# Optimization experiments

Measured on AMD Instinct MI355X. Metric: run time of the kernel, lower is better.

## Reference

```python
import jax, jax.numpy as jnp
import numpy as np

B, S, D, H = 2, 2048, 2048, 16
HD = D // H  # 128


def setup_inputs() -> dict:
    key = jax.random.key(0)
    ks = jax.random.split(key, 5)
    scale = 0.02
    return {
        "hidden_states": jax.random.normal(ks[0], (B, S, D), dtype=jnp.float32),
        "Wqkv_w": jax.random.normal(ks[1], (3 * D, D), dtype=jnp.float32) * scale,
        "Wqkv_b": jax.random.normal(ks[2], (3 * D,), dtype=jnp.float32) * scale,
        "out_w": jax.random.normal(ks[3], (D, D), dtype=jnp.float32) * scale,
        "out_b": jax.random.normal(ks[4], (D,), dtype=jnp.float32) * scale,
    }


def reference(hidden_states, Wqkv_w, Wqkv_b, out_w, out_b):
    b, s, d = hidden_states.shape
    # QKV projection (torch Linear: x @ W.T + b)
    qkv = hidden_states @ Wqkv_w.T + Wqkv_b          # [b, s, 3d]
    qkv = qkv.reshape(b, s, 3, H, HD)                 # 'b s (three h d)'
    q, k, v = qkv[:, :, 0], qkv[:, :, 1], qkv[:, :, 2]  # [b, s, h, hd]
    softmax_scale = 1.0 / np.float32(np.sqrt(HD))
    # full quadratic scores, matching the naive baddbmm path
    scores = jnp.einsum('bthd,bshd->bhts', q, k) * softmax_scale  # [b,h,t,s]
    # causal=False (module default), dropout_p=0.0 -> no mask, no dropout
    attn = jax.nn.softmax(scores, axis=-1)
    ctx = jnp.einsum('bhts,bshd->bthd', attn, v)      # [b, t, h, hd]
    ctx = ctx.reshape(b, s, d)
    return ctx @ out_w.T + out_b
```

## Files before the change

### kernel.cpp

```cpp
#include <hip/hip_runtime.h>
#include <cstdint>
#include <cstddef>

#define B_ 2
#define S_ 2048
#define D_ 2048
#define H_ 16
#define HD_ 128
#define NTOK 4096
#define NQKV 6144

typedef unsigned short u16;
typedef __attribute__((ext_vector_type(8))) __bf16 bf16x8;
typedef __attribute__((ext_vector_type(4))) float f32x4;

__device__ __forceinline__ u16 f2bf(float f) {
  uint32_t u = __builtin_bit_cast(uint32_t, f);
  u = (u + 0x7FFFu + ((u >> 16) & 1u)) >> 16;
  return (u16)u;
}

__device__ __forceinline__ void gload_lds16(const void* g, void* l) {
  __builtin_amdgcn_global_load_lds(
      (const __attribute__((address_space(1))) void*)g,
      (__attribute__((address_space(3))) void*)l, 16, 0, 0);
}

__global__ void cvt_all(const float* __restrict__ hs, const float* __restrict__ wqkv,
                        const float* __restrict__ wo,
                        u16* __restrict__ hsb, u16* __restrict__ wqkvb,
                        u16* __restrict__ wob) {
  const int n1 = (B_ * S_ * D_) / 8;
  const int n2 = n1 + (NQKV * D_) / 8;
  const int n3 = n2 + (D_ * D_) / 8;
  int idx = blockIdx.x * blockDim.x + threadIdx.x;
  int stride = gridDim.x * blockDim.x;
  for (int i = idx; i < n3; i += stride) {
    const float* src; u16* dst; int j;
    if (i < n1)      { src = hs;   dst = hsb;   j = i; }
    else if (i < n2) { src = wqkv; dst = wqkvb; j = i - n1; }
    else             { src = wo;   dst = wob;   j = i - n2; }
    const float4* s = (const float4*)(src + (size_t)j * 8);
    float4 a = s[0], b = s[1];
    union { u16 u[8]; uint4 v; } o;
    o.u[0] = f2bf(a.x); o.u[1] = f2bf(a.y); o.u[2] = f2bf(a.z); o.u[3] = f2bf(a.w);
    o.u[4] = f2bf(b.x); o.u[5] = f2bf(b.y); o.u[6] = f2bf(b.z); o.u[7] = f2bf(b.w);
    *(uint4*)(dst + (size_t)j * 8) = o.v;
  }
}

#define PH_MID() do { asm volatile("s_barrier" ::: "memory"); \
  __builtin_amdgcn_s_setprio(1); } while (0)
#define PH_END() do { __builtin_amdgcn_s_setprio(0); \
  asm volatile("s_barrier" ::: "memory"); } while (0)
#define PH_END_VM(n) do { __builtin_amdgcn_s_setprio(0); \
  asm volatile("s_waitcnt vmcnt(" #n ")" ::: "memory"); \
  asm volatile("s_barrier" ::: "memory"); } while (0)


#define STA(sl,buf,ko) gload_lds16(aSrc + (size_t)(sl)*64*D_ + (ko), aDst + (buf)*8192  + (sl)*4096)
#define STB(sl,buf,ko) gload_lds16(bSrc + (size_t)(sl)*64*D_ + (ko), bDst + (buf)*12288 + (sl)*4096)

#define LOADB(buf) do { _Pragma("unroll") for (int nf = 0; nf < 3; ++nf) \
  _Pragma("unroll") for (int kk = 0; kk < 2; ++kk) \
    breg[nf][kk] = *(const bf16x8*)(sB + (buf)*12288 + (wn*48 + nf*16 + fr)*64 + ((((kk<<2)|fq)^swz)<<3)); } while (0)
#define LOADA_A(buf,q) do { _Pragma("unroll") for (int mm = 0; mm < 2; ++mm) \
  _Pragma("unroll") for (int kk = 0; kk < 2; ++kk) \
    arA[mm][kk] = *(const bf16x8*)(sA + (buf)*8192 + (wm*64 + ((q)*2+mm)*16 + fr)*64 + ((((kk<<2)|fq)^swz)<<3)); } while (0)
#define LOADA_B(buf,q) do { _Pragma("unroll") for (int mm = 0; mm < 2; ++mm) \
  _Pragma("unroll") for (int kk = 0; kk < 2; ++kk) \
    arB[mm][kk] = *(const bf16x8*)(sA + (buf)*8192 + (wm*64 + ((q)*2+mm)*16 + fr)*64 + ((((kk<<2)|fq)^swz)<<3)); } while (0)
#define MFMA12_A(q) do { _Pragma("unroll") for (int kk = 0; kk < 2; ++kk) \
  _Pragma("unroll") for (int mm = 0; mm < 2; ++mm) \
  _Pragma("unroll") for (int nf = 0; nf < 3; ++nf) \
    acc[(q)*2+mm][nf] = __builtin_amdgcn_mfma_f32_16x16x32_bf16(arA[mm][kk], breg[nf][kk], acc[(q)*2+mm][nf], 0, 0, 0); } while (0)
#define MFMA12_B(q) do { _Pragma("unroll") for (int kk = 0; kk < 2; ++kk) \
  _Pragma("unroll") for (int mm = 0; mm < 2; ++mm) \
  _Pragma("unroll") for (int nf = 0; nf < 3; ++nf) \
    acc[(q)*2+mm][nf] = __builtin_amdgcn_mfma_f32_16x16x32_bf16(arB[mm][kk], breg[nf][kk], acc[(q)*2+mm][nf], 0, 0, 0); } while (0)

__global__ __launch_bounds__(512, 4) void qkv_gemm(
    const u16* __restrict__ hsb, const u16* __restrict__ wb,
    const float* __restrict__ bias,
    u16* __restrict__ qb, u16* __restrict__ kb, u16* __restrict__ vT)
{
  __shared__ alignas(1024) u16 sA[2 * 8192];
  __shared__ alignas(1024) u16 sB[2 * 12288];
  const int tid = threadIdx.x;
  const int lane = tid & 63, wid = tid >> 6;
  const int wm = wid >> 2, wn = wid & 3;
  const int fr = lane & 15, fq = lane >> 4;
  const int swz = fr & 7;
  const int m0 = blockIdx.x * 128, n0 = blockIdx.y * 192;

  const int r8 = tid >> 3, g8 = (tid & 7) ^ (r8 & 7);
  const u16* aSrc = hsb + (size_t)(m0 + r8) * D_ + g8 * 8;
  const u16* bSrc = wb  + (size_t)(n0 + r8) * D_ + g8 * 8;
  u16* aDst = sA + wid * 512;
  u16* bDst = sB + wid * 512;

  f32x4 acc[4][3];
  f32x4 z = {0.f, 0.f, 0.f, 0.f};
#pragma unroll
  for (int m = 0; m < 4; ++m)
#pragma unroll
    for (int n = 0; n < 3; ++n) acc[m][n] = z;

  bf16x8 breg[3][2], arA[2][2], arB[2][2];

  STB(0,0,0); STB(1,0,0); STB(2,0,0); STA(0,0,0); STA(1,0,0);
  STB(0,1,64); STB(1,1,64); STB(2,1,64);
  asm volatile("s_waitcnt vmcnt(3)" ::: "memory");
  asm volatile("s_barrier" ::: "memory");

#pragma unroll 1
  for (int j = 0; j < 15; ++j) {
    const int kA1 = (2*j + 1) * 64;
    const int kB2 = (2*j + 2) * 64;
    const int kB3 = (2*j + 3) * 64;
    LOADB(0); LOADA_A(0,0); LOADA_B(0,1); STA(0,1,kA1); STA(1,1,kA1);
      PH_MID(); MFMA12_A(0); PH_END();
    STB(0,0,kB2); STB(1,0,kB2); STB(2,0,kB2);
      PH_MID(); MFMA12_B(1); PH_END_VM(3);
    LOADB(1); LOADA_A(1,0); LOADA_B(1,1); STA(0,0,kB2); STA(1,0,kB2);
      PH_MID(); MFMA12_A(0); PH_END();
    STB(0,1,kB3); STB(1,1,kB3); STB(2,1,kB3);
      PH_MID(); MFMA12_B(1); PH_END_VM(3);
  }
  {
    const int kA31 = 31 * 64;
    LOADB(0); LOADA_A(0,0); LOADA_B(0,1); STA(0,1,kA31); STA(1,1,kA31);
      PH_MID(); MFMA12_A(0); PH_END();
      PH_MID(); MFMA12_B(1); PH_END_VM(0);
    LOADB(1); LOADA_A(1,0); LOADA_B(1,1);
      PH_MID(); MFMA12_A(0); PH_END();
      PH_MID(); MFMA12_B(1); PH_END();
  }

  const float qscale = 0.08838834764831845f;
#pragma unroll
  for (int mf = 0; mf < 4; ++mf)
#pragma unroll
    for (int nf = 0; nf < 3; ++nf) {
      int col = n0 + wn * 48 + nf * 16 + fr;
      float bv = bias[col];
      int t = col >> 11;
      int d2 = col & 2047;
      int h = d2 >> 7, hd = d2 & 127;
#pragma unroll
      for (int r = 0; r < 4; ++r) {
        int row = m0 + wm * 64 + mf * 16 + fq * 4 + r;
        int bb = row >> 11, s = row & 2047;
        int bh = bb * H_ + h;
        float val = acc[mf][nf][r] + bv;
        if (t == 0)      qb[((size_t)bh * S_ + s) * HD_ + hd] = f2bf(val * qscale);
        else if (t == 1) kb[((size_t)bh * S_ + s) * HD_ + hd] = f2bf(val);
        else             vT[((size_t)bh * HD_ + hd) * S_ + s] = f2bf(val);
      }
    }
}


#define OSTA(sl,buf,ko) gload_lds16(aSrcO + (size_t)(sl)*64*D_ + (ko), aDstO + (buf)*8192 + (sl)*4096)
#define OSTB(sl,buf,ko) gload_lds16(bSrcO + (size_t)(sl)*64*D_ + (ko), bDstO + (buf)*8192 + (sl)*4096)

#define OLOADB(buf) do { _Pragma("unroll") for (int nf = 0; nf < 2; ++nf) \
  _Pragma("unroll") for (int kk = 0; kk < 2; ++kk) \
    obreg[nf][kk] = *(const bf16x8*)(sB + (buf)*8192 + (wn*32 + nf*16 + fr)*64 + ((((kk<<2)|fq)^swz)<<3)); } while (0)
#define OLOADA_A(buf,q) do { _Pragma("unroll") for (int mm = 0; mm < 2; ++mm) \
  _Pragma("unroll") for (int kk = 0; kk < 2; ++kk) \
    oarA[mm][kk] = *(const bf16x8*)(sA + (buf)*8192 + (wm*64 + ((q)*2+mm)*16 + fr)*64 + ((((kk<<2)|fq)^swz)<<3)); } while (0)
#define OLOADA_B(buf,q) do { _Pragma("unroll") for (int mm = 0; mm < 2; ++mm) \
  _Pragma("unroll") for (int kk = 0; kk < 2; ++kk) \
    oarB[mm][kk] = *(const bf16x8*)(sA + (buf)*8192 + (wm*64 + ((q)*2+mm)*16 + fr)*64 + ((((kk<<2)|fq)^swz)<<3)); } while (0)
#define OMFMA8_A(q) do { _Pragma("unroll") for (int kk = 0; kk < 2; ++kk) \
  _Pragma("unroll") for (int mm = 0; mm < 2; ++mm) \
  _Pragma("unroll") for (int nf = 0; nf < 2; ++nf) \
    acc[(q)*2+mm][nf] = __builtin_amdgcn_mfma_f32_16x16x32_bf16(oarA[mm][kk], obreg[nf][kk], acc[(q)*2+mm][nf], 0, 0, 0); } while (0)
#define OMFMA8_B(q) do { _Pragma("unroll") for (int kk = 0; kk < 2; ++kk) \
  _Pragma("unroll") for (int mm = 0; mm < 2; ++mm) \
  _Pragma("unroll") for (int nf = 0; nf < 2; ++nf) \
    acc[(q)*2+mm][nf] = __builtin_amdgcn_mfma_f32_16x16x32_bf16(oarB[mm][kk], obreg[nf][kk], acc[(q)*2+mm][nf], 0, 0, 0); } while (0)

__global__ __launch_bounds__(512, 4) void out_gemm(
    const u16* __restrict__ ctx, const u16* __restrict__ wo,
    const float* __restrict__ bias, float* __restrict__ out)
{
  __shared__ alignas(1024) u16 sA[2 * 8192];
  __shared__ alignas(1024) u16 sB[2 * 8192];
  const int tid = threadIdx.x;
  const int lane = tid & 63, wid = tid >> 6;
  const int wm = wid >> 2, wn = wid & 3;
  const int fr = lane & 15, fq = lane >> 4;
  const int swz = fr & 7;
  const int m0 = blockIdx.x * 128, n0 = blockIdx.y * 128;

  const int r8 = tid >> 3, g8 = (tid & 7) ^ (r8 & 7);
  const u16* aSrcO = ctx + (size_t)(m0 + r8) * D_ + g8 * 8;
  const u16* bSrcO = wo  + (size_t)(n0 + r8) * D_ + g8 * 8;
  u16* aDstO = sA + wid * 512;
  u16* bDstO = sB + wid * 512;

  f32x4 acc[4][2];
  f32x4 z = {0.f, 0.f, 0.f, 0.f};
#pragma unroll
  for (int m = 0; m < 4; ++m)
#pragma unroll
    for (int n = 0; n < 2; ++n) acc[m][n] = z;

  bf16x8 obreg[2][2], oarA[2][2], oarB[2][2];

  OSTB(0,0,0); OSTB(1,0,0); OSTA(0,0,0); OSTA(1,0,0);
  OSTB(0,1,64); OSTB(1,1,64);
  asm volatile("s_waitcnt vmcnt(2)" ::: "memory");
  asm volatile("s_barrier" ::: "memory");

#pragma unroll 1
  for (int j = 0; j < 15; ++j) {
    const int kA1 = (2*j + 1) * 64;
    const int kB2 = (2*j + 2) * 64;
    const int kB3 = (2*j + 3) * 64;
    OLOADB(0); OLOADA_A(0,0); OLOADA_B(0,1); OSTA(0,1,kA1); OSTA(1,1,kA1);
      PH_MID(); OMFMA8_A(0); PH_END();
    OSTB(0,0,kB2); OSTB(1,0,kB2);
      PH_MID(); OMFMA8_B(1); PH_END_VM(2);
    OLOADB(1); OLOADA_A(1,0); OLOADA_B(1,1); OSTA(0,0,kB2); OSTA(1,0,kB2);
      PH_MID(); OMFMA8_A(0); PH_END();
    OSTB(0,1,kB3); OSTB(1,1,kB3);
      PH_MID(); OMFMA8_B(1); PH_END_VM(2);
  }
  {
    const int kA31 = 31 * 64;
    OLOADB(0); OLOADA_A(0,0); OLOADA_B(0,1); OSTA(0,1,kA31); OSTA(1,1,kA31);
      PH_MID(); OMFMA8_A(0); PH_END();
      PH_MID(); OMFMA8_B(1); PH_END_VM(0);
    OLOADB(1); OLOADA_A(1,0); OLOADA_B(1,1);
      PH_MID(); OMFMA8_A(0); PH_END();
      PH_MID(); OMFMA8_B(1); PH_END();
  }

#pragma unroll
  for (int mf = 0; mf < 4; ++mf)
#pragma unroll
    for (int nf = 0; nf < 2; ++nf) {
      int col = n0 + wn * 32 + nf * 16 + fr;
      float bv = bias[col];
#pragma unroll
      for (int r = 0; r < 4; ++r) {
        int row = m0 + wm * 64 + mf * 16 + fq * 4 + r;
        out[(size_t)row * D_ + col] = acc[mf][nf][r] + bv;
      }
    }
}

#define STAGEKV(kvv, buf) do { _Pragma("unroll") \
  for (int i = 0; i < 4; ++i) { \
    int lk = i * 256 + tid; int rk = lk >> 4, sk = lk & 15; \
    gload_lds16(Kg + (size_t)((kvv) + rk) * HD_ + ((sk ^ (rk & 7)) << 3), \
                &Kl[buf][i * 2048 + wid * 512]); \
    int rv = lk >> 3, sv = lk & 7; \
    gload_lds16(Vg + (size_t)rv * S_ + (kvv) + ((sv ^ (rv & 7)) << 3), \
                &Vl[buf][i * 2048 + wid * 512]); \
  } } while (0)

__global__ __launch_bounds__(256, 2) void attn(
    const u16* __restrict__ qb, const u16* __restrict__ kb,
    const u16* __restrict__ vT, u16* __restrict__ ctx)
{
  __shared__ alignas(1024) u16 Kl[2][64 * 128];
  __shared__ alignas(1024) u16 Vl[2][128 * 64];
  __shared__ alignas(16) u16 Pl[4][32 * 64];

  const int tid = threadIdx.x, lane = tid & 63, wid = tid >> 6;
  const int fr = lane & 15, fq = lane >> 4;
  const int bh = blockIdx.y;
  const int q0 = blockIdx.x * 128 + wid * 32;
  f32x4 z = {0.f, 0.f, 0.f, 0.f};

  const u16* Kg = kb + (size_t)bh * S_ * HD_;
  const u16* Vg = vT + (size_t)bh * HD_ * S_;

  STAGEKV(0, 0);

  const u16* qbase = qb + ((size_t)bh * S_ + q0) * HD_;
  bf16x8 qa[2][4];
#pragma unroll
  for (int h = 0; h < 2; ++h)
#pragma unroll
    for (int kc = 0; kc < 4; ++kc)
      qa[h][kc] = *(const bf16x8*)(qbase + (size_t)(h * 16 + fr) * HD_ + kc * 32 + fq * 8);

  f32x4 accv[2][8];
#pragma unroll
  for (int h = 0; h < 2; ++h)
#pragma unroll
    for (int n = 0; n < 8; ++n) accv[h][n] = z;
  float m_run[2] = {-1e30f, -1e30f};
  float l_run[2] = {0.f, 0.f};

  __syncthreads();
  int cur = 0;

  for (int kv = 0; kv < S_; kv += 64) {
    if (kv + 64 < S_) STAGEKV(kv + 64, cur ^ 1);

    const u16* Kc = Kl[cur];
    const u16* Vc = Vl[cur];

    f32x4 sc[2][4];
    __builtin_amdgcn_s_setprio(1);
#pragma unroll
    for (int j = 0; j < 4; ++j) {
      f32x4 s0 = z, s1 = z;
#pragma unroll
      for (int kc = 0; kc < 4; ++kc) {
        int row = j * 16 + fr;
        bf16x8 kf = *(const bf16x8*)&Kc[row * 128 + ((kc * 32 + fq * 8) ^ ((row & 7) << 3))];
        s0 = __builtin_amdgcn_mfma_f32_16x16x32_bf16(kf, qa[0][kc], s0, 0, 0, 0);
        s1 = __builtin_amdgcn_mfma_f32_16x16x32_bf16(kf, qa[1][kc], s1, 0, 0, 0);
      }
      sc[0][j] = s0; sc[1][j] = s1;
    }
    __builtin_amdgcn_s_setprio(0);

    float pmax[2];
#pragma unroll
    for (int h = 0; h < 2; ++h) {
      float mx = sc[h][0][0];
#pragma unroll
      for (int j = 0; j < 4; ++j)
#pragma unroll
        for (int r = 0; r < 4; ++r) mx = fmaxf(mx, sc[h][j][r]);
      mx = fmaxf(mx, __shfl_xor(mx, 16));
      mx = fmaxf(mx, __shfl_xor(mx, 32));
      pmax[h] = mx;
    }

    int need = (pmax[0] > m_run[0] + 8.f) || (pmax[1] > m_run[1] + 8.f);
    if (__any(need)) {
#pragma unroll
      for (int h = 0; h < 2; ++h) {
        float mn = fmaxf(m_run[h], pmax[h]);
        float corr = __expf(m_run[h] - mn);
        m_run[h] = mn;
        l_run[h] *= corr;
#pragma unroll
        for (int r = 0; r < 4; ++r) {
          float rc = __shfl(corr, (lane & 48) | (fq * 4 + r));
#pragma unroll
          for (int n = 0; n < 8; ++n) accv[h][n][r] *= rc;
        }
      }
    }

    u16* Pw = Pl[wid];
#pragma unroll
    for (int h = 0; h < 2; ++h) {
      float ls = 0.f;
#pragma unroll
      for (int j = 0; j < 4; ++j) {
        union { u16 u[4]; ushort4 v; } pk;
#pragma unroll
        for (int r = 0; r < 4; ++r) {
          float p = __expf(sc[h][j][r] - m_run[h]);
          ls += p;
          pk.u[r] = f2bf(p);
        }
        int prow = h * 16 + fr;
        *(ushort4*)&Pw[prow * 64 + ((j * 16 + fq * 4) ^ ((fr & 7) << 3))] = pk.v;
      }
      ls += __shfl_xor(ls, 16);
      ls += __shfl_xor(ls, 32);
      l_run[h] += ls;
    }

    __builtin_amdgcn_s_setprio(1);
#pragma unroll
    for (int kc = 0; kc < 2; ++kc) {
      int pcol = (kc * 32 + fq * 8) ^ ((fr & 7) << 3);
      bf16x8 pa0 = *(const bf16x8*)&Pw[fr * 64 + pcol];
      bf16x8 pa1 = *(const bf16x8*)&Pw[(16 + fr) * 64 + pcol];
#pragma unroll
      for (int n = 0; n < 8; ++n) {
        int row = n * 16 + fr;
        bf16x8 vf = *(const bf16x8*)&Vc[row * 64 + ((kc * 32 + fq * 8) ^ ((row & 7) << 3))];
        accv[0][n] = __builtin_amdgcn_mfma_f32_16x16x32_bf16(pa0, vf, accv[0][n], 0, 0, 0);
        accv[1][n] = __builtin_amdgcn_mfma_f32_16x16x32_bf16(pa1, vf, accv[1][n], 0, 0, 0);
      }
    }
    __builtin_amdgcn_s_setprio(0);

    __syncthreads();
    cur ^= 1;
  }

  float inv[2][4];
#pragma unroll
  for (int h = 0; h < 2; ++h)
#pragma unroll
    for (int r = 0; r < 4; ++r) {
      float l = __shfl(l_run[h], (lane & 48) | (fq * 4 + r));
      inv[h][r] = 1.f / l;
    }
  u16* cb = ctx + (((size_t)(bh >> 4)) * S_ + q0) * D_ + (size_t)(bh & 15) * HD_;
#pragma unroll
  for (int h = 0; h < 2; ++h)
#pragma unroll
    for (int n = 0; n < 8; ++n)
#pragma unroll
      for (int r = 0; r < 4; ++r) {
        int q = h * 16 + fq * 4 + r;
        cb[(size_t)q * D_ + n * 16 + fr] = f2bf(accv[h][n][r] * inv[h][r]);
      }
}

extern "C" void kernel_launch(void* const* d_in, const int* in_sizes, int n_in,
                              void* d_out, int out_size, void* d_ws, size_t ws_size,
                              hipStream_t stream) {
  const float* hs   = (const float*)d_in[0];
  const float* wqkv = (const float*)d_in[1];
  const float* bqkv = (const float*)d_in[2];
  const float* wo   = (const float*)d_in[3];
  const float* bo   = (const float*)d_in[4];
  float* out = (float*)d_out;

  char* ws = (char*)d_ws;
  u16* hsb   = (u16*)(ws);
  u16* wqkvb = (u16*)(ws + 16777216);
  u16* wob   = (u16*)(ws + 41943040);
  u16* qb    = (u16*)(ws + 50331648);
  u16* kb    = (u16*)(ws + 67108864);
  u16* vT    = (u16*)(ws + 83886080);
  u16* ctx   = (u16*)(ws + 100663296);

  cvt_all<<<2048, 256, 0, stream>>>(hs, wqkv, wo, hsb, wqkvb, wob);

  qkv_gemm<<<dim3(NTOK / 128, NQKV / 192), 512, 0, stream>>>(hsb, wqkvb, bqkv, qb, kb, vT);
  attn<<<dim3(S_ / 128, B_ * H_), 256, 0, stream>>>(qb, kb, vT, ctx);
  out_gemm<<<dim3(NTOK / 128, D_ / 128), 512, 0, stream>>>(ctx, wob, bo, out);
}
```

Measured before the change: 286.8 us.

## Software-pipeline attention loop to overlap QK^T of next tile with softmax/PV

```diff
diff --git a/kernel.cpp b/kernel.cpp
--- a/kernel.cpp
+++ b/kernel.cpp
@@ -160,7 +160,6 @@
     }
 }
 
-
 #define OSTA(sl,buf,ko) gload_lds16(aSrcO + (size_t)(sl)*64*D_ + (ko), aDstO + (buf)*8192 + (sl)*4096)
 #define OSTB(sl,buf,ko) gload_lds16(bSrcO + (size_t)(sl)*64*D_ + (ko), bDstO + (buf)*8192 + (sl)*4096)
 
@@ -253,15 +252,85 @@
     }
 }
 
-#define STAGEKV(kvv, buf) do { _Pragma("unroll") \
+#define SK(kvv, buf) do { _Pragma("unroll") \
   for (int i = 0; i < 4; ++i) { \
     int lk = i * 256 + tid; int rk = lk >> 4, sk = lk & 15; \
     gload_lds16(Kg + (size_t)((kvv) + rk) * HD_ + ((sk ^ (rk & 7)) << 3), \
                 &Kl[buf][i * 2048 + wid * 512]); \
-    int rv = lk >> 3, sv = lk & 7; \
+  } } while (0)
+#define SV(kvv, buf) do { _Pragma("unroll") \
+  for (int i = 0; i < 4; ++i) { \
+    int lk = i * 256 + tid; int rv = lk >> 3, sv = lk & 7; \
     gload_lds16(Vg + (size_t)rv * S_ + (kvv) + ((sv ^ (rv & 7)) << 3), \
                 &Vl[buf][i * 2048 + wid * 512]); \
   } } while (0)
+
+#define QKT(scX, Kc) do { \
+  __builtin_amdgcn_s_setprio(1); \
+  _Pragma("unroll") for (int j = 0; j < 4; ++j) { \
+    f32x4 s0 = z, s1 = z; \
+    _Pragma("unroll") for (int kc = 0; kc < 4; ++kc) { \
+      int row = j * 16 + fr; \
+      bf16x8 kf = *(const bf16x8*)&(Kc)[row * 128 + ((kc * 32 + fq * 8) ^ ((row & 7) << 3))]; \
+      s0 = __builtin_amdgcn_mfma_f32_16x16x32_bf16(kf, qa[0][kc], s0, 0, 0, 0); \
+      s1 = __builtin_amdgcn_mfma_f32_16x16x32_bf16(kf, qa[1][kc], s1, 0, 0, 0); \
+    } \
+    scX[0][j] = s0; scX[1][j] = s1; \
+  } \
+  __builtin_amdgcn_s_setprio(0); } while (0)
+
+#define FINISH(scX, Vc) do { \
+  float pmax[2]; \
+  _Pragma("unroll") for (int h = 0; h < 2; ++h) { \
+    float mx = scX[h][0][0]; \
+    _Pragma("unroll") for (int j = 0; j < 4; ++j) \
+      _Pragma("unroll") for (int r = 0; r < 4; ++r) mx = fmaxf(mx, scX[h][j][r]); \
+    mx = fmaxf(mx, __shfl_xor(mx, 16)); \
+    mx = fmaxf(mx, __shfl_xor(mx, 32)); \
+    pmax[h] = mx; \
+  } \
+  int need = (pmax[0] > m_run[0] + 8.f) || (pmax[1] > m_run[1] + 8.f); \
+  if (__any(need)) { \
+    _Pragma("unroll") for (int h = 0; h < 2; ++h) { \
+      float mn = fmaxf(m_run[h], pmax[h]); \
+      float corr = __expf(m_run[h] - mn); \
+      m_run[h] = mn; \
+      l_run[h] *= corr; \
+      _Pragma("unroll") for (int r = 0; r < 4; ++r) { \
+        float rc = __shfl(corr, (lane & 48) | (fq * 4 + r)); \
+        _Pragma("unroll") for (int n = 0; n < 8; ++n) accv[h][n][r] *= rc; \
+      } \
+    } \
+  } \
+  _Pragma("unroll") for (int h = 0; h < 2; ++h) { \
+    float ls = 0.f; \
+    _Pragma("unroll") for (int j = 0; j < 4; ++j) { \
+      union { u16 u[4]; ushort4 v; } pk; \
+      _Pragma("unroll") for (int r = 0; r < 4; ++r) { \
+        float p = __expf(scX[h][j][r] - m_run[h]); \
+        ls += p; \
+        pk.u[r] = f2bf(p); \
+      } \
+      int prow = h * 16 + fr; \
+      *(ushort4*)&Pw[prow * 64 + ((j * 16 + fq * 4) ^ ((fr & 7) << 3))] = pk.v; \
+    } \
+    ls += __shfl_xor(ls, 16); \
+    ls += __shfl_xor(ls, 32); \
+    l_run[h] += ls; \
+  } \
+  __builtin_amdgcn_s_setprio(1); \
+  _Pragma("unroll") for (int kc = 0; kc < 2; ++kc) { \
+    int pcol = (kc * 32 + fq * 8) ^ ((fr & 7) << 3); \
+    bf16x8 pa0 = *(const bf16x8*)&Pw[fr * 64 + pcol]; \
+    bf16x8 pa1 = *(const bf16x8*)&Pw[(16 + fr) * 64 + pcol]; \
+    _Pragma("unroll") for (int n = 0; n < 8; ++n) { \
+      int row = n * 16 + fr; \
+      bf16x8 vf = *(const bf16x8*)&(Vc)[row * 64 + ((kc * 32 + fq * 8) ^ ((row & 7) << 3))]; \
+      accv[0][n] = __builtin_amdgcn_mfma_f32_16x16x32_bf16(pa0, vf, accv[0][n], 0, 0, 0); \
+      accv[1][n] = __builtin_amdgcn_mfma_f32_16x16x32_bf16(pa1, vf, accv[1][n], 0, 0, 0); \
+    } \
+  } \
+  __builtin_amdgcn_s_setprio(0); } while (0)
 
 __global__ __launch_bounds__(256, 2) void attn(
     const u16* __restrict__ qb, const u16* __restrict__ kb,
@@ -279,8 +348,9 @@
 
   const u16* Kg = kb + (size_t)bh * S_ * HD_;
   const u16* Vg = vT + (size_t)bh * HD_ * S_;
-
-  STAGEKV(0, 0);
+  u16* Pw = Pl[wid];
+
+  SK(0, 0);
 
   const u16* qbase = qb + ((size_t)bh * S_ + q0) * HD_;
   bf16x8 qa[2][4];
@@ -298,100 +368,32 @@
   float m_run[2] = {-1e30f, -1e30f};
   float l_run[2] = {0.f, 0.f};
 
+  f32x4 scA[2][4], scB[2][4];
+
   __syncthreads();
-  int cur = 0;
-
-  for (int kv = 0; kv < S_; kv += 64) {
-    if (kv + 64 < S_) STAGEKV(kv + 64, cur ^ 1);
-
-    const u16* Kc = Kl[cur];
-    const u16* Vc = Vl[cur];
-
-    f32x4 sc[2][4];
-    __builtin_amdgcn_s_setprio(1);
-#pragma unroll
-    for (int j = 0; j < 4; ++j) {
-      f32x4 s0 = z, s1 = z;
-#pragma unroll
-      for (int kc = 0; kc < 4; ++kc) {
-        int row = j * 16 + fr;
-        bf16x8 kf = *(const bf16x8*)&Kc[row * 128 + ((kc * 32 + fq * 8) ^ ((row & 7) << 3))];
-        s0 = __builtin_amdgcn_mfma_f32_16x16x32_bf16(kf, qa[0][kc], s0, 0, 0, 0);
-        s1 = __builtin_amdgcn_mfma_f32_16x16x32_bf16(kf, qa[1][kc], s1, 0, 0, 0);
-      }
-      sc[0][j] = s0; sc[1][j] = s1;
-    }
-    __builtin_amdgcn_s_setprio(0);
-
-    float pmax[2];
-#pragma unroll
-    for (int h = 0; h < 2; ++h) {
-      float mx = sc[h][0][0];
-#pragma unroll
-      for (int j = 0; j < 4; ++j)
-#pragma unroll
-        for (int r = 0; r < 4; ++r) mx = fmaxf(mx, sc[h][j][r]);
-      mx = fmaxf(mx, __shfl_xor(mx, 16));
-      mx = fmaxf(mx, __shfl_xor(mx, 32));
-      pmax[h] = mx;
-    }
-
-    int need = (pmax[0] > m_run[0] + 8.f) || (pmax[1] > m_run[1] + 8.f);
-    if (__any(need)) {
-#pragma unroll
-      for (int h = 0; h < 2; ++h) {
-        float mn = fmaxf(m_run[h], pmax[h]);
-        float corr = __expf(m_run[h] - mn);
-        m_run[h] = mn;
-        l_run[h] *= corr;
-#pragma unroll
-        for (int r = 0; r < 4; ++r) {
-          float rc = __shfl(corr, (lane & 48) | (fq * 4 + r));
-#pragma unroll
-          for (int n = 0; n < 8; ++n) accv[h][n][r] *= rc;
-        }
-      }
-    }
-
-    u16* Pw = Pl[wid];
-#pragma unroll
-    for (int h = 0; h < 2; ++h) {
-      float ls = 0.f;
-#pragma unroll
-      for (int j = 0; j < 4; ++j) {
-        union { u16 u[4]; ushort4 v; } pk;
-#pragma unroll
-        for (int r = 0; r < 4; ++r) {
-          float p = __expf(sc[h][j][r] - m_run[h]);
-          ls += p;
-          pk.u[r] = f2bf(p);
-        }
-        int prow = h * 16 + fr;
-        *(ushort4*)&Pw[prow * 64 + ((j * 16 + fq * 4) ^ ((fr & 7) << 3))] = pk.v;
-      }
-      ls += __shfl_xor(ls, 16);
-      ls += __shfl_xor(ls, 32);
-      l_run[h] += ls;
-    }
-
-    __builtin_amdgcn_s_setprio(1);
-#pragma unroll
-    for (int kc = 0; kc < 2; ++kc) {
-      int pcol = (kc * 32 + fq * 8) ^ ((fr & 7) << 3);
-      bf16x8 pa0 = *(const bf16x8*)&Pw[fr * 64 + pcol];
-      bf16x8 pa1 = *(const bf16x8*)&Pw[(16 + fr) * 64 + pcol];
-#pragma unroll
-      for (int n = 0; n < 8; ++n) {
-        int row = n * 16 + fr;
-        bf16x8 vf = *(const bf16x8*)&Vc[row * 64 + ((kc * 32 + fq * 8) ^ ((row & 7) << 3))];
-        accv[0][n] = __builtin_amdgcn_mfma_f32_16x16x32_bf16(pa0, vf, accv[0][n], 0, 0, 0);
-        accv[1][n] = __builtin_amdgcn_mfma_f32_16x16x32_bf16(pa1, vf, accv[1][n], 0, 0, 0);
-      }
-    }
-    __builtin_amdgcn_s_setprio(0);
-
+  SK(64, 1); SV(0, 0);
+  QKT(scA, Kl[0]);
+  __syncthreads();
+
+#pragma unroll 1
+  for (int j = 0; j < 15; ++j) {
+    const int t1 = 2 * j + 1;
+    SK((t1 + 1) * 64, 0); SV(t1 * 64, 1);
+    QKT(scB, Kl[1]);
+    FINISH(scA, Vl[0]);
     __syncthreads();
-    cur ^= 1;
+    const int t2 = 2 * j + 2;
+    SK((t2 + 1) * 64, 1); SV(t2 * 64, 0);
+    QKT(scA, Kl[0]);
+    FINISH(scB, Vl[1]);
+    __syncthreads();
+  }
+  {
+    SV(31 * 64, 1);
+    QKT(scB, Kl[1]);
+    FINISH(scA, Vl[0]);
+    __syncthreads();
+    FINISH(scB, Vl[1]);
   }
 
   float inv[2][4];
```

Measured after the change: 288.2 us. Within noise of the previous version (+0.5%).
